# Performance work log

Hardware: AMD Instinct MI355X
Metric: run time of the kernel (lower is better)

Reference implementation:

```python
import jax, jax.numpy as jnp
from jax import lax
import numpy as np

KERNEL_SIZE = 5
GROUP_SIZE = 40
GMAX = 160                      # g sampled in [0, GMAX)
MAX_ITERS = (GMAX - 1) // GROUP_SIZE   # static upper bound on |g|//group_size = 3
B = 4096
D = 8192


def _circ_conv(x, k):
    # x: [1, B, D], k: [B, K] -> grouped (depthwise) circular conv1d, groups=B
    pad = KERNEL_SIZE - 1
    left = pad // 2
    xp = jnp.pad(x, ((0, 0), (0, 0), (left, pad - left)), mode='wrap')
    return lax.conv_general_dilated(
        xp, k[:, None, :], window_strides=(1,), padding='VALID',
        feature_group_count=k.shape[0], dimension_numbers=('NCH', 'OIH', 'NCH'))


def setup_inputs() -> dict:
    key = jax.random.key(0)
    k1, k2, k3 = jax.random.split(key, 3)
    x = jax.random.normal(k1, (B, D), dtype=jnp.float32)
    g = jax.random.randint(k2, (B,), 0, GMAX, dtype=jnp.int32)
    kernels = jax.random.normal(k3, (2 * GROUP_SIZE + 1, KERNEL_SIZE), dtype=jnp.float32)
    return {"x": x, "g": g, "kernels": kernels}


def reference(x, g, kernels):
    G = GROUP_SIZE
    xc = x[None]                          # [1, B, D]  (x.view(-1,1,D).permute(1,0,2))
    sign = jnp.sign(g)                    # [B]
    iters = jnp.abs(g) // G               # [B] data-dependent per-sample loop count
    max_it = jnp.max(iters)               # dynamic max over the batch
    max_k = kernels[sign * G + G]         # [B, K]
    id_k = kernels[G]                     # [K] learned 'identity' kernel
    # true delta kernel: exact no-op under circular pad, used for steps past max_it
    delta = jnp.zeros((KERNEL_SIZE,), x.dtype).at[(KERNEL_SIZE - 1) // 2].set(1.0)

    h = xc
    for i in range(MAX_ITERS):            # static bound; delta makes extra steps no-ops
        inactive = jnp.where(i < max_it, id_k, delta)          # [K]
        k_i = jnp.where((i < iters)[:, None], max_k, inactive[None, :])  # [B, K]
        h = _circ_conv(h, k_i)
    rem = jnp.abs(g) % G
    fin_k = kernels[rem * sign + G]       # [B, K]
    out = _circ_conv(h, fin_k)            # [1, B, D]
    return jnp.transpose(out, (1, 0, 2))  # [B, 1, D]
```

## Files before the change

kernel.cpp:

```cpp
#include <hip/hip_runtime.h>

#define BB 4096
#define DD 8192
#define KK 5
#define GS 40
#define MAXIT 3
#define EFF 17
#define DF4 (DD/4)
#define EPAD 20
#define WS_OFF 64

typedef float vf4 __attribute__((ext_vector_type(4)));

__device__ __forceinline__ int iabs(int a) { return a < 0 ? -a : a; }

template<int LEN>
__device__ __forceinline__ void compose5(float* e, const float* k5) {
    float ne[LEN + KK - 1];
#pragma unroll
    for (int m = 0; m < LEN + KK - 1; ++m) ne[m] = 0.f;
#pragma unroll
    for (int m = 0; m < LEN; ++m)
#pragma unroll
        for (int j = 0; j < KK; ++j) ne[m + j] += e[m] * k5[j];
#pragma unroll
    for (int m = 0; m < LEN + KK - 1; ++m) e[m] = ne[m];
}

__device__ __forceinline__ void pick5(int i, int iters, int max_it,
                                      const float* maxk, const float* idk,
                                      float* k5) {
#pragma unroll
    for (int j = 0; j < KK; ++j)
        k5[j] = (i < iters) ? maxk[j]
              : ((i < max_it) ? idk[j] : ((j == (KK - 1) / 2) ? 1.f : 0.f));
}

__global__ __launch_bounds__(256) void k_compose(const int* __restrict__ g,
                                                 const float* __restrict__ kernels,
                                                 float* __restrict__ wsE) {
    __shared__ int red[256];
    const int t = threadIdx.x;

    const int4* g4 = (const int4*)g;
    int m = 0;
    for (int i = t; i < BB / 4; i += 256) {
        int4 v = g4[i];
        m = max(m, max(max(iabs(v.x), iabs(v.y)), max(iabs(v.z), iabs(v.w))));
    }
    red[t] = m;
    __syncthreads();
    for (int s = 128; s > 0; s >>= 1) {
        if (t < s) red[t] = max(red[t], red[t + s]);
        __syncthreads();
    }
    const int max_it = red[0] / GS;

    const int r  = blockIdx.x * 256 + t;
    const int gv = g[r];
    const int sign  = gv > 0 ? 1 : (gv < 0 ? -1 : 0);
    const int a     = iabs(gv);
    const int iters = a / GS;
    const int rem   = a % GS;

    const float* mk = kernels + (size_t)(sign * GS + GS) * KK;
    const float* ik = kernels + (size_t)GS * KK;
    const float* fk = kernels + (size_t)(rem * sign + GS) * KK;
    float maxk[KK], idk[KK], fink[KK];
#pragma unroll
    for (int j = 0; j < KK; ++j) { maxk[j] = mk[j]; idk[j] = ik[j]; fink[j] = fk[j]; }

    float e[EPAD];
#pragma unroll
    for (int q = 0; q < EPAD; ++q) e[q] = 0.f;
    e[0] = 1.f;

    float k5[KK];
    pick5(0, iters, max_it, maxk, idk, k5); compose5<1>(e, k5);
    pick5(1, iters, max_it, maxk, idk, k5); compose5<5>(e, k5);
    pick5(2, iters, max_it, maxk, idk, k5); compose5<9>(e, k5);
    compose5<13>(e, fink);

    vf4* dst = (vf4*)(wsE + (size_t)r * EPAD);
    vf4 o0; o0.x = e[0];  o0.y = e[1];  o0.z = e[2];  o0.w = e[3];
    vf4 o1; o1.x = e[4];  o1.y = e[5];  o1.z = e[6];  o1.w = e[7];
    vf4 o2; o2.x = e[8];  o2.y = e[9];  o2.z = e[10]; o2.w = e[11];
    vf4 o3; o3.x = e[12]; o3.y = e[13]; o3.z = e[14]; o3.w = e[15];
    vf4 o4; o4.x = e[16]; o4.y = e[17]; o4.z = e[18]; o4.w = e[19];
    dst[0] = o0; dst[1] = o1; dst[2] = o2; dst[3] = o3; dst[4] = o4;
}

__global__ __launch_bounds__(256) void k_conv_direct(const float* __restrict__ x,
                                                     const float* __restrict__ wsE,
                                                     float* __restrict__ out) {
    const int b = blockIdx.x;
    const int t = threadIdx.x;

    const float4* ev = (const float4*)(wsE + (size_t)b * EPAD);
    float4 e0 = ev[0], e1 = ev[1], e2 = ev[2], e3 = ev[3], e4 = ev[4];
    float e[EFF] = { e0.x, e0.y, e0.z, e0.w,
                     e1.x, e1.y, e1.z, e1.w,
                     e2.x, e2.y, e2.z, e2.w,
                     e3.x, e3.y, e3.z, e3.w,
                     e4.x };

    const float4* xr   = (const float4*)(x + (size_t)b * DD);
    float4*       outr = (float4*)(out + (size_t)b * DD);

#pragma unroll 2
    for (int k = 0; k < 8; ++k) {
        const int v = k * 256 + t;
        float f[EFF + 3];
#pragma unroll
        for (int q = 0; q < 5; ++q) {
            float4 val = xr[(v - 2 + q) & (DF4 - 1)];
            f[q * 4 + 0] = val.x; f[q * 4 + 1] = val.y;
            f[q * 4 + 2] = val.z; f[q * 4 + 3] = val.w;
        }
        float oc[4];
#pragma unroll
        for (int c = 0; c < 4; ++c) {
            float s = 0.f;
#pragma unroll
            for (int m = 0; m < EFF; ++m) s += e[m] * f[c + m];
            oc[c] = s;
        }
        float4 o;
        o.x = oc[0]; o.y = oc[1]; o.z = oc[2]; o.w = oc[3];
        outr[v] = o;
    }
}

__global__ __launch_bounds__(256) void k_max_it(const int* __restrict__ g,
                                                int* __restrict__ ws) {
    __shared__ int red[256];
    int t = threadIdx.x;
    int m = 0;
    for (int i = t; i < BB; i += 256) m = max(m, iabs(g[i]));
    red[t] = m;
    __syncthreads();
    for (int s = 128; s > 0; s >>= 1) {
        if (t < s) red[t] = max(red[t], red[t + s]);
        __syncthreads();
    }
    if (t == 0) ws[0] = red[0] / GS;
}

__global__ __launch_bounds__(256) void k_conv_fb(const float* __restrict__ x,
                                                 const int* __restrict__ g,
                                                 const float* __restrict__ kernels,
                                                 const int* __restrict__ ws,
                                                 float* __restrict__ out) {
    const int b = blockIdx.x;
    const int t = threadIdx.x;

    const int gv    = g[b];
    const int sign  = gv > 0 ? 1 : (gv < 0 ? -1 : 0);
    const int a     = iabs(gv);
    const int iters = a / GS;
    const int rem   = a % GS;
    const int max_it = ws[0];

    float maxk[KK], idk[KK], fink[KK];
    const float* mk = kernels + (size_t)(sign * GS + GS) * KK;
    const float* ik = kernels + (size_t)GS * KK;
    const float* fk = kernels + (size_t)(rem * sign + GS) * KK;
#pragma unroll
    for (int j = 0; j < KK; ++j) { maxk[j] = mk[j]; idk[j] = ik[j]; fink[j] = fk[j]; }

    float e[EPAD];
#pragma unroll
    for (int q = 0; q < EPAD; ++q) e[q] = 0.f;
    e[0] = 1.f;
    float k5[KK];
    pick5(0, iters, max_it, maxk, idk, k5); compose5<1>(e, k5);
    pick5(1, iters, max_it, maxk, idk, k5); compose5<5>(e, k5);
    pick5(2, iters, max_it, maxk, idk, k5); compose5<9>(e, k5);
    compose5<13>(e, fink);

    const float4* xr   = (const float4*)(x + (size_t)b * DD);
    float4*       outr = (float4*)(out + (size_t)b * DD);
#pragma unroll 2
    for (int k = 0; k < 8; ++k) {
        const int v = k * 256 + t;
        float f[EFF + 3];
#pragma unroll
        for (int q = 0; q < 5; ++q) {
            float4 val = xr[(v - 2 + q) & (DF4 - 1)];
            f[q * 4 + 0] = val.x; f[q * 4 + 1] = val.y;
            f[q * 4 + 2] = val.z; f[q * 4 + 3] = val.w;
        }
        float oc[4];
#pragma unroll
        for (int c = 0; c < 4; ++c) {
            float s = 0.f;
#pragma unroll
            for (int m = 0; m < EFF; ++m) s += e[m] * f[c + m];
            oc[c] = s;
        }
        float4 o;
        o.x = oc[0]; o.y = oc[1]; o.z = oc[2]; o.w = oc[3];
        outr[v] = o;
    }
}

extern "C" void kernel_launch(void* const* d_in, const int* in_sizes, int n_in,
                              void* d_out, int out_size, void* d_ws, size_t ws_size,
                              hipStream_t stream) {
    const float* x       = (const float*)d_in[0];
    const int*   g       = (const int*)d_in[1];
    const float* kernels = (const float*)d_in[2];
    float*       out     = (float*)d_out;

    const size_t need = (size_t)(WS_OFF + BB * EPAD) * sizeof(float);
    if (ws_size >= need) {
        float* wsE = (float*)d_ws + WS_OFF;
        k_compose<<<BB / 256, 256, 0, stream>>>(g, kernels, wsE);
        k_conv_direct<<<BB, 256, 0, stream>>>(x, wsE, out);
    } else {
        int* ws = (int*)d_ws;
        k_max_it<<<1, 256, 0, stream>>>(g, ws);
        k_conv_fb<<<BB, 256, 0, stream>>>(x, g, kernels, ws, out);
    }
}
```

Measured before the change: 277.5 us.

## Stage row chunks in LDS via direct global-to-LDS loads, nontemporal stores

The convolution kernel now splits each row into four 2048-float chunks, one per 128-thread block. Each block copies its chunk plus a 2-float4 wrapped halo on each side into shared memory using global_load_lds, with the last four halo vectors loaded normally. Each thread then reads its five overlapping float4 windows from LDS rather than issuing five overlapping global loads, and writes results with nontemporal stores. The aim is to cut redundant global and cache traffic and keep output writes from polluting the cache. The cost is a block barrier, LDS use, and reliance on the async LDS-load builtin's wave-uniform addressing behaving correctly.

```diff
diff --git a/kernel.cpp b/kernel.cpp
--- a/kernel.cpp
+++ b/kernel.cpp
@@ -6,13 +6,22 @@
 #define GS 40
 #define MAXIT 3
 #define EFF 17
+#define CHUNK 2048
+#define C4 (CHUNK/4)
 #define DF4 (DD/4)
+#define TPB 128
 #define EPAD 20
 #define WS_OFF 64
 
 typedef float vf4 __attribute__((ext_vector_type(4)));
 
 __device__ __forceinline__ int iabs(int a) { return a < 0 ? -a : a; }
+
+__device__ __forceinline__ void gload_lds16(const float4* g, float4* l) {
+    __builtin_amdgcn_global_load_lds(
+        (const __attribute__((address_space(1))) void*)g,
+        (__attribute__((address_space(3))) void*)l, 16, 0, 0);
+}
 
 template<int LEN>
 __device__ __forceinline__ void compose5(float* e, const float* k5) {
@@ -90,11 +99,28 @@
     dst[0] = o0; dst[1] = o1; dst[2] = o2; dst[3] = o3; dst[4] = o4;
 }
 
-__global__ __launch_bounds__(256) void k_conv_direct(const float* __restrict__ x,
-                                                     const float* __restrict__ wsE,
-                                                     float* __restrict__ out) {
-    const int b = blockIdx.x;
-    const int t = threadIdx.x;
+__global__ __launch_bounds__(TPB) void k_conv_pre(const float* __restrict__ x,
+                                                  const float* __restrict__ wsE,
+                                                  float* __restrict__ out) {
+    __shared__ float4 ldsw[C4 + 4];
+
+    const int bi   = blockIdx.x;
+    const int b    = bi >> 2;
+    const int ch   = bi & 3;
+    const int t    = threadIdx.x;
+    const int c0f4 = ch * C4;
+
+    const float4* xr = (const float4*)(x + (size_t)b * DD);
+
+#pragma unroll
+    for (int s = 0; s < 4; ++s) {
+        const int wi = s * TPB + t;
+        gload_lds16(xr + ((c0f4 - 2 + wi) & (DF4 - 1)), &ldsw[wi]);
+    }
+    if (t < 4) {
+        const int wi = 512 + t;
+        ldsw[wi] = xr[(c0f4 - 2 + wi) & (DF4 - 1)];
+    }
 
     const float4* ev = (const float4*)(wsE + (size_t)b * EPAD);
     float4 e0 = ev[0], e1 = ev[1], e2 = ev[2], e3 = ev[3], e4 = ev[4];
@@ -104,30 +130,30 @@
                      e3.x, e3.y, e3.z, e3.w,
                      e4.x };
 
-    const float4* xr   = (const float4*)(x + (size_t)b * DD);
-    float4*       outr = (float4*)(out + (size_t)b * DD);
-
-#pragma unroll 2
-    for (int k = 0; k < 8; ++k) {
-        const int v = k * 256 + t;
+    __syncthreads();
+
+    vf4* outr = (vf4*)(out + (size_t)b * DD);
+#pragma unroll
+    for (int s = 0; s < 4; ++s) {
+        const int v = s * TPB + t;
         float f[EFF + 3];
 #pragma unroll
         for (int q = 0; q < 5; ++q) {
-            float4 val = xr[(v - 2 + q) & (DF4 - 1)];
+            float4 val = ldsw[v + q];
             f[q * 4 + 0] = val.x; f[q * 4 + 1] = val.y;
             f[q * 4 + 2] = val.z; f[q * 4 + 3] = val.w;
         }
         float oc[4];
 #pragma unroll
         for (int c = 0; c < 4; ++c) {
-            float s = 0.f;
-#pragma unroll
-            for (int m = 0; m < EFF; ++m) s += e[m] * f[c + m];
-            oc[c] = s;
-        }
-        float4 o;
+            float s2 = 0.f;
+#pragma unroll
+            for (int m = 0; m < EFF; ++m) s2 += e[m] * f[c + m];
+            oc[c] = s2;
+        }
+        vf4 o;
         o.x = oc[0]; o.y = oc[1]; o.z = oc[2]; o.w = oc[3];
-        outr[v] = o;
+        __builtin_nontemporal_store(o, outr + c0f4 + v);
     }
 }
 
@@ -216,7 +242,7 @@
     if (ws_size >= need) {
         float* wsE = (float*)d_ws + WS_OFF;
         k_compose<<<BB / 256, 256, 0, stream>>>(g, kernels, wsE);
-        k_conv_direct<<<BB, 256, 0, stream>>>(x, wsE, out);
+        k_conv_pre<<<BB * (DD / CHUNK), TPB, 0, stream>>>(x, wsE, out);
     } else {
         int* ws = (int*)d_ws;
         k_max_it<<<1, 256, 0, stream>>>(g, ws);
```

Result: faster. 240.1 us (-13.5%).

## Stage per-wave x windows in LDS and split rows across four blocks

Applied to the files above, without the earlier changes.

Replaces the direct conv kernel with a version where each wavefront loads its 128-float4 slice plus halo once into shared memory and reads neighbouring float4s from LDS rather than issuing five overlapping global loads per output. Each row is split across four blocks (16384 blocks total) with launch bounds for higher occupancy, and output uses nontemporal stores. The intent is to cut redundant global/L2 traffic and improve memory-level parallelism. It relies on a wave-local s_waitcnt instead of a barrier, which assumes each wave only reads its own LDS region.

```diff
diff --git a/kernel.cpp b/kernel.cpp
--- a/kernel.cpp
+++ b/kernel.cpp
@@ -90,11 +90,25 @@
     dst[0] = o0; dst[1] = o1; dst[2] = o2; dst[3] = o3; dst[4] = o4;
 }
 
-__global__ __launch_bounds__(256) void k_conv_direct(const float* __restrict__ x,
-                                                     const float* __restrict__ wsE,
-                                                     float* __restrict__ out) {
-    const int b = blockIdx.x;
-    const int t = threadIdx.x;
+__global__ __launch_bounds__(256, 8) void k_conv_wave(const float* __restrict__ x,
+                                                      const float* __restrict__ wsE,
+                                                      float* __restrict__ out) {
+    __shared__ float4 win[4][132];
+
+    const int bi  = blockIdx.x;
+    const int b   = bi >> 2;
+    const int ch  = bi & 3;
+    const int t   = threadIdx.x;
+    const int w   = t >> 6;
+    const int l   = t & 63;
+    const int wf0 = ch * 512 + w * 128;
+
+    const float4* xr = (const float4*)(x + (size_t)b * DD);
+
+    float4 r0 = xr[(wf0 -  2 + l) & (DF4 - 1)];
+    float4 r1 = xr[(wf0 + 62 + l) & (DF4 - 1)];
+    float4 rt;
+    if (l < 4) rt = xr[(wf0 + 126 + l) & (DF4 - 1)];
 
     const float4* ev = (const float4*)(wsE + (size_t)b * EPAD);
     float4 e0 = ev[0], e1 = ev[1], e2 = ev[2], e3 = ev[3], e4 = ev[4];
@@ -104,16 +118,20 @@
                      e3.x, e3.y, e3.z, e3.w,
                      e4.x };
 
-    const float4* xr   = (const float4*)(x + (size_t)b * DD);
-    float4*       outr = (float4*)(out + (size_t)b * DD);
-
-#pragma unroll 2
-    for (int k = 0; k < 8; ++k) {
-        const int v = k * 256 + t;
+    win[w][l]      = r0;
+    win[w][64 + l] = r1;
+    if (l < 4) win[w][128 + l] = rt;
+
+    asm volatile("s_waitcnt lgkmcnt(0)" ::: "memory");
+
+    vf4* outr = (vf4*)(out + (size_t)b * DD);
+
+    {
         float f[EFF + 3];
-#pragma unroll
-        for (int q = 0; q < 5; ++q) {
-            float4 val = xr[(v - 2 + q) & (DF4 - 1)];
+        f[0] = r0.x; f[1] = r0.y; f[2] = r0.z; f[3] = r0.w;
+#pragma unroll
+        for (int q = 1; q < 5; ++q) {
+            float4 val = win[w][l + q];
             f[q * 4 + 0] = val.x; f[q * 4 + 1] = val.y;
             f[q * 4 + 2] = val.z; f[q * 4 + 3] = val.w;
         }
@@ -125,9 +143,29 @@
             for (int m = 0; m < EFF; ++m) s += e[m] * f[c + m];
             oc[c] = s;
         }
-        float4 o;
-        o.x = oc[0]; o.y = oc[1]; o.z = oc[2]; o.w = oc[3];
-        outr[v] = o;
+        vf4 o; o.x = oc[0]; o.y = oc[1]; o.z = oc[2]; o.w = oc[3];
+        __builtin_nontemporal_store(o, outr + wf0 + l);
+    }
+
+    {
+        float f[EFF + 3];
+        f[0] = r1.x; f[1] = r1.y; f[2] = r1.z; f[3] = r1.w;
+#pragma unroll
+        for (int q = 1; q < 5; ++q) {
+            float4 val = win[w][64 + l + q];
+            f[q * 4 + 0] = val.x; f[q * 4 + 1] = val.y;
+            f[q * 4 + 2] = val.z; f[q * 4 + 3] = val.w;
+        }
+        float oc[4];
+#pragma unroll
+        for (int c = 0; c < 4; ++c) {
+            float s = 0.f;
+#pragma unroll
+            for (int m = 0; m < EFF; ++m) s += e[m] * f[c + m];
+            oc[c] = s;
+        }
+        vf4 o; o.x = oc[0]; o.y = oc[1]; o.z = oc[2]; o.w = oc[3];
+        __builtin_nontemporal_store(o, outr + wf0 + 64 + l);
     }
 }
 
@@ -216,7 +254,7 @@
     if (ws_size >= need) {
         float* wsE = (float*)d_ws + WS_OFF;
         k_compose<<<BB / 256, 256, 0, stream>>>(g, kernels, wsE);
-        k_conv_direct<<<BB, 256, 0, stream>>>(x, wsE, out);
+        k_conv_wave<<<BB * 4, 256, 0, stream>>>(x, wsE, out);
     } else {
         int* ws = (int*)d_ws;
         k_max_it<<<1, 256, 0, stream>>>(g, ws);
```

New measurement: 237.3 us. -14.5%, faster.
